# Optimization experiments

Hardware: AMD Instinct MI355X
Metric: run time of the kernel (lower is better)

Reference implementation:

```python
import jax, jax.numpy as jnp
import numpy as np

WS = 8           # window_size
OV = 4           # overlap = int(window_size * overlap_ratio)
OS = WS + 2 * OV # overlap_size = 16
NH = 6           # num_heads
EPS = 1e-5


def setup_inputs() -> dict:
    key = jax.random.key(0)
    ks = jax.random.split(key, 5)
    B, C, H, W = 4, 192, 256, 256
    s = 0.02
    return {
        "x": jax.random.normal(ks[0], (B, C, H, W), jnp.float32),
        "norm_gamma": jnp.ones((C,), jnp.float32),
        "norm_beta": jnp.zeros((C,), jnp.float32),
        "Wq": s * jax.random.normal(ks[1], (C, C), jnp.float32),
        "bq": jnp.zeros((C,), jnp.float32),
        "Wkv": s * jax.random.normal(ks[2], (C, 2 * C), jnp.float32),
        "bkv": jnp.zeros((2 * C,), jnp.float32),
        "Wo": s * jax.random.normal(ks[3], (C, C), jnp.float32),
        "bo": jnp.zeros((C,), jnp.float32),
    }


def reference(x, norm_gamma, norm_beta, Wq, bq, Wkv, bkv, Wo, bo):
    B, C, H, W = x.shape
    hd = C // NH
    scale = hd ** (-0.5)
    nHw, nWw = H // WS, W // WS
    nW = nHw * nWw

    residual = x
    xn = jnp.transpose(x, (0, 2, 3, 1))  # (B,H,W,C)
    mu = xn.mean(-1, keepdims=True)
    var = xn.var(-1, keepdims=True)
    ln = (xn - mu) * jax.lax.rsqrt(var + EPS) * norm_gamma + norm_beta  # (B,H,W,C)

    # --- queries: non-overlapping windows (window_partition) ---
    q_win = ln.reshape(B, nHw, WS, nWw, WS, C)
    q_win = jnp.transpose(q_win, (0, 1, 3, 2, 4, 5)).reshape(B * nW, WS * WS, C)
    q = q_win @ Wq + bq  # (N, ws^2, C)

    # --- keys/values: overlapping patches (Unfold equivalent) ---
    xp = jnp.pad(ln, ((0, 0), (OV, OV), (OV, OV), (0, 0)))  # (B,H+2ov,W+2ov,C)
    ih = (jnp.arange(nHw) * WS)[:, None] + jnp.arange(OS)[None, :]  # (nHw, OS)
    iw = (jnp.arange(nWw) * WS)[:, None] + jnp.arange(OS)[None, :]  # (nWw, OS)
    # (B, nHw, nWw, OS, OS, C)
    patches = xp[:, ih[:, None, :, None], iw[None, :, None, :], :]
    kv_in = patches.reshape(B * nW, OS * OS, C)
    kv = kv_in @ Wkv + bkv  # (N, os^2, 2C)
    k, v = kv[..., :C], kv[..., C:]

    # --- multi-head attention per window ---
    qh = q.reshape(-1, WS * WS, NH, hd).transpose(0, 2, 1, 3)   # (N,nh,q,hd)
    kh = k.reshape(-1, OS * OS, NH, hd).transpose(0, 2, 1, 3)   # (N,nh,kv,hd)
    vh = v.reshape(-1, OS * OS, NH, hd).transpose(0, 2, 1, 3)
    attn = jax.nn.softmax(jnp.einsum("nhqd,nhkd->nhqk", qh * scale, kh), axis=-1)
    out = jnp.einsum("nhqk,nhkd->nhqd", attn, vh)
    out = out.transpose(0, 2, 1, 3).reshape(-1, WS * WS, C)
    out = out @ Wo + bo

    # --- window_reverse + residual ---
    out = out.reshape(B, nHw, nWw, WS, WS, C)
    out = jnp.transpose(out, (0, 1, 3, 2, 4, 5)).reshape(B, H, W, C)
    return jnp.transpose(out, (0, 3, 1, 2)) + residual
```

## Files before the change

kernel.cpp:

```cpp
#include <hip/hip_runtime.h>
#include <hip/hip_bf16.h>

typedef __bf16 bf16;
typedef __bf16 bf16x8 __attribute__((ext_vector_type(8)));
typedef float f32x4 __attribute__((ext_vector_type(4)));
typedef unsigned int u32x2 __attribute__((ext_vector_type(2)));
typedef unsigned int u32x4 __attribute__((ext_vector_type(4)));

#define DEVI static __device__ __forceinline__

static constexpr int Bn = 4, Cc = 192, Hh = 256, Wd = 256;
static constexpr int NHd = 6, HD = 32;
static constexpr int Mtot = Bn * Hh * Wd;
static constexpr float EPSv = 1e-5f;
static constexpr float SCQ = 0.2550629072427404f;

DEVI f32x4 mfma16(bf16x8 a, bf16x8 b, f32x4 c) {
    return __builtin_amdgcn_mfma_f32_16x16x32_bf16(a, b, c, 0, 0, 0);
}

DEVI f32x4 mfma16f8(long long a, long long b, f32x4 c) {
    return __builtin_amdgcn_mfma_f32_16x16x32_fp8_fp8(a, b, c, 0, 0, 0);
}

template <bool HIGH>
DEVI unsigned cvtpk_fp8(float lo, float hi, unsigned old) {
    return (unsigned)__builtin_amdgcn_cvt_pk_fp8_f32(lo, hi, (int)old, HIGH);
}

__global__ __launch_bounds__(256) void k_prep(const float* Wq, const float* Wkv,
                                              const float* Wo, bf16* WT,
                                              unsigned char* WoT8) {
    int idx = blockIdx.x * 256 + threadIdx.x;
    if (idx < 576 * 192) {
        int n = idx / 192, k = idx % 192;
        float v = (n < 192) ? Wq[k * 192 + n] * SCQ : Wkv[k * 384 + (n - 192)];
        WT[idx] = (bf16)v;
    } else if (idx < 576 * 192 + 192 * 192) {
        int j = idx - 576 * 192;
        int n = j / 192, k = j % 192;
        float w = Wo[k * 192 + n];
        WoT8[j] = (unsigned char)(cvtpk_fp8<false>(w, w, 0u) & 0xFFu);
    }
}

__global__ __launch_bounds__(256) void k_lnqkv(const float* __restrict__ x,
                                               const float* __restrict__ gamma,
                                               const float* __restrict__ beta,
                                               const bf16* __restrict__ WT,
                                               const float* __restrict__ bq,
                                               const float* __restrict__ bkv,
                                               unsigned char* __restrict__ QKV8) {
    constexpr int AS = 200;
    __shared__ __align__(16) bf16 A[64 * AS];
    __shared__ float red[2][4][64];
    __shared__ float sg[Cc], sbv[Cc];

    int tid = threadIdx.x;
    int q = tid >> 6, p = tid & 63;
    int base = blockIdx.x * 64;
    int b = base >> 16;
    int hw = base & 65535;
    int h = hw >> 8, w0 = hw & 255;
    if (tid < Cc) { sg[tid] = gamma[tid]; sbv[tid] = beta[tid]; }

    const float* xb = x + ((size_t)(b * Cc + q * 48) * Hh + h) * Wd + w0 + p;
    float xv[48];
#pragma unroll
    for (int i = 0; i < 48; ++i) xv[i] = xb[(size_t)i * Hh * Wd];
    float s = 0.f, s2 = 0.f;
#pragma unroll
    for (int i = 0; i < 48; ++i) { s += xv[i]; s2 += xv[i] * xv[i]; }
    red[0][q][p] = s; red[1][q][p] = s2;
    __syncthreads();
    float mu = (red[0][0][p] + red[0][1][p] + red[0][2][p] + red[0][3][p]) * (1.f / 192.f);
    float m2 = (red[1][0][p] + red[1][1][p] + red[1][2][p] + red[1][3][p]) * (1.f / 192.f);
    float rs = rsqrtf(m2 - mu * mu + EPSv);
#pragma unroll
    for (int i0 = 0; i0 < 48; i0 += 8) {
        bf16x8 o;
#pragma unroll
        for (int j = 0; j < 8; ++j) {
            int c = q * 48 + i0 + j;
            o[j] = (bf16)((xv[i0 + j] - mu) * rs * sg[c] + sbv[c]);
        }
        *(bf16x8*)&A[p * AS + q * 48 + i0] = o;
    }
    __syncthreads();

    int lane = tid & 63, l15 = lane & 15, g = lane >> 4;
    const bf16* Wbase = WT + (size_t)(q * 144 + l15) * Cc + g * 8;
#pragma unroll 1
    for (int nt = 0; nt < 9; ++nt) {
        f32x4 acc[4] = {};
        const bf16* wp = Wbase + (size_t)nt * 16 * Cc;
#pragma unroll
        for (int kk = 0; kk < 6; ++kk) {
            bf16x8 wb = *(const bf16x8*)(wp + kk * 32);
#pragma unroll
            for (int mt = 0; mt < 4; ++mt) {
                bf16x8 a = *(bf16x8*)&A[(mt * 16 + l15) * AS + kk * 32 + g * 8];
                acc[mt] = mfma16(wb, a, acc[mt]);
            }
        }
        int n0 = q * 144 + nt * 16 + g * 4;
        const float* bsrc = (n0 < 192) ? (bq + n0) : (bkv + n0 - 192);
        f32x4 b4 = *(const f32x4*)bsrc;
        if (n0 < 192) b4 *= SCQ;
        unsigned char* outp = QKV8 + (size_t)(n0 >> 5) * Mtot * HD + (n0 & 31);
#pragma unroll
        for (int mt = 0; mt < 4; ++mt) {
            unsigned pk = 0;
            pk = cvtpk_fp8<false>(acc[mt][0] + b4[0], acc[mt][1] + b4[1], pk);
            pk = cvtpk_fp8<true>(acc[mt][2] + b4[2], acc[mt][3] + b4[3], pk);
            *(unsigned*)(outp + (size_t)(base + mt * 16 + l15) * HD) = pk;
        }
    }
}

__global__ __launch_bounds__(128) void k_attn(const unsigned char* __restrict__ QKV8,
                                              const float* __restrict__ bkv,
                                              unsigned char* __restrict__ AO8) {
    constexpr int VS = 264;
    int bid = blockIdx.x;
    bid = (bid & 7) * 3072 + (bid >> 3);
    int head = bid >> 12;
    int win = bid & 4095;
    int b = win >> 10, wloc = win & 1023;
    int h0 = ((wloc >> 5) << 3), w0 = ((wloc & 31) << 3);
    bool interior = (h0 != 0) && (h0 != Hh - 8) && (w0 != 0) && (w0 != Wd - 8);

    int tid = threadIdx.x, wave = tid >> 6, lane = tid & 63;
    int l15 = lane & 15, g = lane >> 4;

    const unsigned char* Qh = QKV8 + (size_t)head * Mtot * HD;
    const unsigned char* Kh = QKV8 + (size_t)(6 + head) * Mtot * HD;
    const unsigned char* Vh = QKV8 + (size_t)(12 + head) * Mtot * HD;
    unsigned char* Oh = AO8 + (size_t)head * Mtot * HD;
    long long p00 = (long long)(b * Hh + h0 - 4) * Wd + (w0 - 4);

    __shared__ __align__(16) unsigned char VT8[32 * VS];

#pragma unroll
    for (int rr = 0; rr < 2; ++rr) {
        int r = tid + rr * 128;
        unsigned wv[8];
        if (interior) {
            const unsigned char* vr = Vh + (p00 + (r >> 4) * Wd + (r & 15)) * HD;
            u32x4 a0 = *(const u32x4*)(vr);
            u32x4 a1 = *(const u32x4*)(vr + 16);
#pragma unroll
            for (int w = 0; w < 4; ++w) { wv[w] = a0[w]; wv[w + 4] = a1[w]; }
        } else {
            int ph = h0 - 4 + (r >> 4), pw = w0 - 4 + (r & 15);
            bool ok = ((unsigned)ph < (unsigned)Hh) && ((unsigned)pw < (unsigned)Wd);
            long long pix = ok ? ((long long)(b * Hh + ph) * Wd + pw) : 0;
            const unsigned char* vr = Vh + pix * HD;
            u32x4 a0 = *(const u32x4*)(vr);
            u32x4 a1 = *(const u32x4*)(vr + 16);
            const float* vb = bkv + Cc + head * HD;
#pragma unroll
            for (int w = 0; w < 8; ++w) {
                unsigned bw = 0;
                bw = cvtpk_fp8<false>(vb[4 * w], vb[4 * w + 1], bw);
                bw = cvtpk_fp8<true>(vb[4 * w + 2], vb[4 * w + 3], bw);
                unsigned lw = (w < 4) ? a0[w] : a1[w - 4];
                wv[w] = ok ? lw : bw;
            }
        }
#pragma unroll
        for (int w = 0; w < 8; ++w) {
            unsigned word = wv[w];
            VT8[(4 * w + 0) * VS + r] = (unsigned char)(word);
            VT8[(4 * w + 1) * VS + r] = (unsigned char)(word >> 8);
            VT8[(4 * w + 2) * VS + r] = (unsigned char)(word >> 16);
            VT8[(4 * w + 3) * VS + r] = (unsigned char)(word >> 24);
        }
    }

    int qrA = wave * 32 + l15;
    int qrB = qrA + 16;
    size_t qpixA = (size_t)(b * Hh + h0 + (qrA >> 3)) * Wd + w0 + (qrA & 7);
    size_t qpixB = (size_t)(b * Hh + h0 + (qrB >> 3)) * Wd + w0 + (qrB & 7);
    long long aqA = *(const long long*)(Qh + qpixA * HD + g * 8);
    long long aqB = *(const long long*)(Qh + qpixB * HD + g * 8);
    __syncthreads();

    const f32x4 z = {0.f, 0.f, 0.f, 0.f};
    const unsigned char* kp = Kh + (p00 + l15) * HD + g * 8;
    float sa0 = 0.f, sa1 = 0.f, sa2 = 0.f, sa3 = 0.f;
    float sb0 = 0.f, sb1 = 0.f, sb2 = 0.f, sb3 = 0.f;
    unsigned pkA[16], pkB[16];
    long long kb = 0;
    bool colok = true;
    if (!interior) {
        unsigned kb0 = 0, kb1 = 0;
        const float* kbp = bkv + head * HD + g * 8;
        kb0 = cvtpk_fp8<false>(kbp[0], kbp[1], kb0);
        kb0 = cvtpk_fp8<true>(kbp[2], kbp[3], kb0);
        kb1 = cvtpk_fp8<false>(kbp[4], kbp[5], kb1);
        kb1 = cvtpk_fp8<true>(kbp[6], kbp[7], kb1);
        kb = (long long)(((unsigned long long)kb1 << 32) | kb0);
        colok = ((unsigned)(w0 - 4 + l15) < (unsigned)Wd);
    }
#pragma unroll 1
    for (int c = 0; c < 4; ++c) {
        f32x4 sA[4], sB[4];
        __builtin_amdgcn_s_setprio(1);
        if (interior) {
#pragma unroll
            for (int u = 0; u < 4; ++u) {
                long long kf = *(const long long*)(kp + (size_t)(c * 4 + u) * Wd * HD);
                sA[u] = mfma16f8(kf, aqA, z);
                sB[u] = mfma16f8(kf, aqB, z);
            }
        } else {
#pragma unroll
            for (int u = 0; u < 4; ++u) {
                int t = c * 4 + u;
                int ph = h0 - 4 + t;
                long long kf;
                if ((unsigned)ph < (unsigned)Hh) {
                    kf = *(const long long*)(kp + (size_t)t * Wd * HD);
                    kf = colok ? kf : kb;
                } else {
                    kf = kb;
                }
                sA[u] = mfma16f8(kf, aqA, z);
                sB[u] = mfma16f8(kf, aqB, z);
            }
        }
        __builtin_amdgcn_s_setprio(0);
#pragma unroll
        for (int u = 0; u < 4; ++u) {
            float a0 = __builtin_amdgcn_exp2f(sA[u][0]);
            float a1 = __builtin_amdgcn_exp2f(sA[u][1]);
            float a2 = __builtin_amdgcn_exp2f(sA[u][2]);
            float a3 = __builtin_amdgcn_exp2f(sA[u][3]);
            sa0 += a0; sa1 += a1; sa2 += a2; sa3 += a3;
            unsigned wA = 0;
            wA = cvtpk_fp8<false>(a0, a1, wA);
            wA = cvtpk_fp8<true>(a2, a3, wA);
            pkA[c * 4 + u] = wA;
            float b0 = __builtin_amdgcn_exp2f(sB[u][0]);
            float b1 = __builtin_amdgcn_exp2f(sB[u][1]);
            float b2 = __builtin_amdgcn_exp2f(sB[u][2]);
            float b3 = __builtin_amdgcn_exp2f(sB[u][3]);
            sb0 += b0; sb1 += b1; sb2 += b2; sb3 += b3;
            unsigned wB = 0;
            wB = cvtpk_fp8<false>(b0, b1, wB);
            wB = cvtpk_fp8<true>(b2, b3, wB);
            pkB[c * 4 + u] = wB;
        }
    }
    float sumA = (sa0 + sa1) + (sa2 + sa3);
    sumA += __shfl_xor(sumA, 16);
    sumA += __shfl_xor(sumA, 32);
    float invA = __builtin_amdgcn_rcpf(sumA);
    float sumB = (sb0 + sb1) + (sb2 + sb3);
    sumB += __shfl_xor(sumB, 16);
    sumB += __shfl_xor(sumB, 32);
    float invB = __builtin_amdgcn_rcpf(sumB);

    int srcA = l15 | ((2 * (g & 1)) << 4);
    int srcB = srcA + 16;
    bool ghi = (g >> 1) != 0;
#define PV_EPILOGUE(PK, INV, JT)                                                        \
    {                                                                                   \
        f32x4 o0 = z, o1 = z;                                                           \
        _Pragma("unroll")                                                               \
        for (int kk = 0; kk < 8; ++kk) {                                                \
            unsigned s0 = __shfl(PK[2 * kk], srcA);                                     \
            unsigned s1 = __shfl(PK[2 * kk + 1], srcA);                                 \
            unsigned s2 = __shfl(PK[2 * kk], srcB);                                     \
            unsigned s3 = __shfl(PK[2 * kk + 1], srcB);                                 \
            unsigned lo = ghi ? s1 : s0;                                                \
            unsigned hi = ghi ? s3 : s2;                                                \
            long long ap = (long long)(((unsigned long long)hi << 32) | lo);            \
            long long bv0 = *(const long long*)&VT8[l15 * VS + kk * 32 + g * 8];        \
            long long bv1 = *(const long long*)&VT8[(16 + l15) * VS + kk * 32 + g * 8]; \
            __builtin_amdgcn_s_setprio(1);                                              \
            o0 = mfma16f8(ap, bv0, o0);                                                 \
            o1 = mfma16f8(ap, bv1, o1);                                                 \
            __builtin_amdgcn_s_setprio(0);                                              \
        }                                                                               \
        float invr[4];                                                                  \
        _Pragma("unroll")                                                               \
        for (int r = 0; r < 4; ++r)                                                     \
            invr[r] = __shfl(INV, (lane & 48) | (g * 4 + r));                           \
        _Pragma("unroll")                                                               \
        for (int r = 0; r < 4; ++r) {                                                   \
            int row = wave * 32 + JT * 16 + g * 4 + r;                                  \
            size_t pix = (size_t)(b * Hh + h0 + (row >> 3)) * Wd + w0 + (row & 7);      \
            float v0 = o0[r] * invr[r];                                                 \
            float v1 = o1[r] * invr[r];                                                 \
            Oh[pix * HD + l15] = (unsigned char)(cvtpk_fp8<false>(v0, v0, 0u) & 0xFFu); \
            Oh[pix * HD + 16 + l15] = (unsigned char)(cvtpk_fp8<false>(v1, v1, 0u) & 0xFFu); \
        }                                                                               \
    }
    PV_EPILOGUE(pkA, invA, 0)
    PV_EPILOGUE(pkB, invB, 1)
#undef PV_EPILOGUE
}

__global__ __launch_bounds__(256) void k_out(const unsigned char* __restrict__ AO8,
                                             const unsigned char* __restrict__ WoT8,
                                             const float* __restrict__ bo,
                                             const float* __restrict__ x,
                                             float* __restrict__ out) {
    int row0 = blockIdx.x * 64;
    int tid = threadIdx.x, wave = tid >> 6, lane = tid & 63;
    int l15 = lane & 15, g = lane >> 4;
    int nb = wave * 48;
    f32x4 acc[4][3] = {};
    const unsigned char* Arow[4];
#pragma unroll
    for (int mt = 0; mt < 4; ++mt) Arow[mt] = AO8 + (size_t)(row0 + mt * 16 + l15) * HD + g * 8;
    const unsigned char* Wrow[3];
#pragma unroll
    for (int nt = 0; nt < 3; ++nt) Wrow[nt] = WoT8 + (size_t)(nb + nt * 16 + l15) * Cc + g * 8;
#pragma unroll
    for (int kk = 0; kk < 6; ++kk) {
        long long a[4];
#pragma unroll
        for (int mt = 0; mt < 4; ++mt)
            a[mt] = *(const long long*)(Arow[mt] + (size_t)kk * Mtot * HD);
#pragma unroll
        for (int nt = 0; nt < 3; ++nt) {
            long long bb = *(const long long*)(Wrow[nt] + kk * 32);
#pragma unroll
            for (int mt = 0; mt < 4; ++mt) acc[mt][nt] = mfma16f8(a[mt], bb, acc[mt][nt]);
        }
    }
    __shared__ float st[192 * 65];
#pragma unroll
    for (int nt = 0; nt < 3; ++nt) {
        float bval = bo[nb + nt * 16 + l15];
#pragma unroll
        for (int mt = 0; mt < 4; ++mt)
#pragma unroll
            for (int r = 0; r < 4; ++r) {
                int ccol = nb + nt * 16 + l15;
                int px = mt * 16 + g * 4 + r;
                st[ccol * 65 + px] = acc[mt][nt][r] + bval;
            }
    }
    __syncthreads();
    int bb2 = row0 / (Hh * Wd);
    int rem = row0 % (Hh * Wd);
    int h = rem / Wd, wstart = rem % Wd;
    for (int idx = tid; idx < 192 * 64; idx += 256) {
        int cc = idx >> 6, px = idx & 63;
        size_t ga = ((size_t)(bb2 * Cc + cc) * Hh + h) * Wd + wstart + px;
        out[ga] = st[cc * 65 + px] + x[ga];
    }
}

extern "C" void kernel_launch(void* const* d_in, const int* in_sizes, int n_in,
                              void* d_out, int out_size, void* d_ws, size_t ws_size,
                              hipStream_t stream) {
    const float* x     = (const float*)d_in[0];
    const float* gamma = (const float*)d_in[1];
    const float* beta  = (const float*)d_in[2];
    const float* Wq    = (const float*)d_in[3];
    const float* bq    = (const float*)d_in[4];
    const float* Wkv   = (const float*)d_in[5];
    const float* bkv   = (const float*)d_in[6];
    const float* Wo    = (const float*)d_in[7];
    const float* bo    = (const float*)d_in[8];
    float* out = (float*)d_out;

    char* ws = (char*)d_ws;
    constexpr size_t P8  = (size_t)Mtot * HD;
    constexpr size_t QKV8SZ = 18 * P8;
    constexpr size_t AO8SZ  = 6 * P8;
    unsigned char* QKV8 = (unsigned char*)(ws);
    unsigned char* AO8  = (unsigned char*)(ws + QKV8SZ);
    bf16*          WT   = (bf16*)(ws + QKV8SZ + AO8SZ);
    unsigned char* WoT8 = (unsigned char*)(ws + QKV8SZ + AO8SZ + 221184);

    k_prep<<<576, 256, 0, stream>>>(Wq, Wkv, Wo, WT, WoT8);
    k_lnqkv<<<Mtot / 64, 256, 0, stream>>>(x, gamma, beta, WT, bq, bkv, QKV8);
    k_attn<<<4096 * NHd, 128, 0, stream>>>(QKV8, bkv, AO8);
    k_out<<<Mtot / 64, 256, 0, stream>>>(AO8, WoT8, bo, x, out);
}
```

Before: 403.5 us.

## Use fp8 MFMA for LN+QKV projection with full-row tiles per block

Switches the LayerNorm+QKV GEMM from bf16 to fp8 MFMA. Weights are pre-scaled by 16 and quantized to fp8, and the normalized activations are stored as fp8 in LDS. Each block now handles a full 256-pixel image row, with one thread computing per-pixel LN statistics over all channels, so the cross-wave reduction is gone and each weight fragment is reused across four times more pixels. The cost is a second read of x for normalization and lower precision for both activations and weights, which risks accuracy. Occupancy also drops because of the larger LDS footprint.

New measurement: 380.0 us. -5.8%, faster.

```diff
diff --git a/kernel.cpp b/kernel.cpp
--- a/kernel.cpp
+++ b/kernel.cpp
@@ -15,10 +15,6 @@
 static constexpr float EPSv = 1e-5f;
 static constexpr float SCQ = 0.2550629072427404f;
 
-DEVI f32x4 mfma16(bf16x8 a, bf16x8 b, f32x4 c) {
-    return __builtin_amdgcn_mfma_f32_16x16x32_bf16(a, b, c, 0, 0, 0);
-}
-
 DEVI f32x4 mfma16f8(long long a, long long b, f32x4 c) {
     return __builtin_amdgcn_mfma_f32_16x16x32_fp8_fp8(a, b, c, 0, 0, 0);
 }
@@ -29,13 +25,14 @@
 }
 
 __global__ __launch_bounds__(256) void k_prep(const float* Wq, const float* Wkv,
-                                              const float* Wo, bf16* WT,
+                                              const float* Wo, unsigned char* WT8,
                                               unsigned char* WoT8) {
     int idx = blockIdx.x * 256 + threadIdx.x;
     if (idx < 576 * 192) {
         int n = idx / 192, k = idx % 192;
-        float v = (n < 192) ? Wq[k * 192 + n] * SCQ : Wkv[k * 384 + (n - 192)];
-        WT[idx] = (bf16)v;
+        float v = (n < 192) ? Wq[k * 192 + n] * (SCQ * 16.f)
+                            : Wkv[k * 384 + (n - 192)] * 16.f;
+        WT8[idx] = (unsigned char)(cvtpk_fp8<false>(v, v, 0u) & 0xFFu);
     } else if (idx < 576 * 192 + 192 * 192) {
         int j = idx - 576 * 192;
         int n = j / 192, k = j % 192;
@@ -47,73 +44,79 @@
 __global__ __launch_bounds__(256) void k_lnqkv(const float* __restrict__ x,
                                                const float* __restrict__ gamma,
                                                const float* __restrict__ beta,
-                                               const bf16* __restrict__ WT,
+                                               const unsigned char* __restrict__ WT8,
                                                const float* __restrict__ bq,
                                                const float* __restrict__ bkv,
                                                unsigned char* __restrict__ QKV8) {
     constexpr int AS = 200;
-    __shared__ __align__(16) bf16 A[64 * AS];
-    __shared__ float red[2][4][64];
-    __shared__ float sg[Cc], sbv[Cc];
+    __shared__ __align__(16) unsigned char A[256 * AS];
 
     int tid = threadIdx.x;
-    int q = tid >> 6, p = tid & 63;
-    int base = blockIdx.x * 64;
-    int b = base >> 16;
-    int hw = base & 65535;
-    int h = hw >> 8, w0 = hw & 255;
-    if (tid < Cc) { sg[tid] = gamma[tid]; sbv[tid] = beta[tid]; }
-
-    const float* xb = x + ((size_t)(b * Cc + q * 48) * Hh + h) * Wd + w0 + p;
-    float xv[48];
-#pragma unroll
-    for (int i = 0; i < 48; ++i) xv[i] = xb[(size_t)i * Hh * Wd];
-    float s = 0.f, s2 = 0.f;
-#pragma unroll
-    for (int i = 0; i < 48; ++i) { s += xv[i]; s2 += xv[i] * xv[i]; }
-    red[0][q][p] = s; red[1][q][p] = s2;
+    int bid = blockIdx.x;
+    int b = bid >> 8, h = bid & 255;
+    const size_t cs = (size_t)Hh * Wd;
+    const float* xb = x + ((size_t)(b * Cc) * Hh + h) * Wd + tid;
+
+    float s0 = 0.f, s1 = 0.f, q0 = 0.f, q1 = 0.f;
+#pragma unroll 8
+    for (int c = 0; c < Cc; c += 2) {
+        float v0 = xb[(size_t)c * cs], v1 = xb[(size_t)(c + 1) * cs];
+        s0 += v0; q0 += v0 * v0;
+        s1 += v1; q1 += v1 * v1;
+    }
+    float mu = (s0 + s1) * (1.f / 192.f);
+    float m2 = (q0 + q1) * (1.f / 192.f);
+    float rs = rsqrtf(m2 - mu * mu + EPSv);
+
+#pragma unroll 4
+    for (int c = 0; c < Cc; c += 4) {
+        float v0 = (xb[(size_t)(c + 0) * cs] - mu) * rs * gamma[c + 0] + beta[c + 0];
+        float v1 = (xb[(size_t)(c + 1) * cs] - mu) * rs * gamma[c + 1] + beta[c + 1];
+        float v2 = (xb[(size_t)(c + 2) * cs] - mu) * rs * gamma[c + 2] + beta[c + 2];
+        float v3 = (xb[(size_t)(c + 3) * cs] - mu) * rs * gamma[c + 3] + beta[c + 3];
+        unsigned pk = 0;
+        pk = cvtpk_fp8<false>(v0, v1, pk);
+        pk = cvtpk_fp8<true>(v2, v3, pk);
+        *(unsigned*)&A[tid * AS + c] = pk;
+    }
     __syncthreads();
-    float mu = (red[0][0][p] + red[0][1][p] + red[0][2][p] + red[0][3][p]) * (1.f / 192.f);
-    float m2 = (red[1][0][p] + red[1][1][p] + red[1][2][p] + red[1][3][p]) * (1.f / 192.f);
-    float rs = rsqrtf(m2 - mu * mu + EPSv);
-#pragma unroll
-    for (int i0 = 0; i0 < 48; i0 += 8) {
-        bf16x8 o;
-#pragma unroll
-        for (int j = 0; j < 8; ++j) {
-            int c = q * 48 + i0 + j;
-            o[j] = (bf16)((xv[i0 + j] - mu) * rs * sg[c] + sbv[c]);
-        }
-        *(bf16x8*)&A[p * AS + q * 48 + i0] = o;
-    }
-    __syncthreads();
-
-    int lane = tid & 63, l15 = lane & 15, g = lane >> 4;
-    const bf16* Wbase = WT + (size_t)(q * 144 + l15) * Cc + g * 8;
+
+    int q = tid >> 6, lane = tid & 63, l15 = lane & 15, g = lane >> 4;
+    const unsigned char* Wbase = WT8 + (size_t)(q * 144 + l15) * Cc + g * 8;
+    size_t pixrow = ((size_t)(b * Hh) + h) * Wd;
 #pragma unroll 1
     for (int nt = 0; nt < 9; ++nt) {
-        f32x4 acc[4] = {};
-        const bf16* wp = Wbase + (size_t)nt * 16 * Cc;
-#pragma unroll
-        for (int kk = 0; kk < 6; ++kk) {
-            bf16x8 wb = *(const bf16x8*)(wp + kk * 32);
-#pragma unroll
-            for (int mt = 0; mt < 4; ++mt) {
-                bf16x8 a = *(bf16x8*)&A[(mt * 16 + l15) * AS + kk * 32 + g * 8];
-                acc[mt] = mfma16(wb, a, acc[mt]);
-            }
-        }
+        long long wf[6];
+        const unsigned char* wp = Wbase + (size_t)nt * 16 * Cc;
+#pragma unroll
+        for (int kk = 0; kk < 6; ++kk) wf[kk] = *(const long long*)(wp + kk * 32);
         int n0 = q * 144 + nt * 16 + g * 4;
         const float* bsrc = (n0 < 192) ? (bq + n0) : (bkv + n0 - 192);
         f32x4 b4 = *(const f32x4*)bsrc;
         if (n0 < 192) b4 *= SCQ;
         unsigned char* outp = QKV8 + (size_t)(n0 >> 5) * Mtot * HD + (n0 & 31);
-#pragma unroll
-        for (int mt = 0; mt < 4; ++mt) {
-            unsigned pk = 0;
-            pk = cvtpk_fp8<false>(acc[mt][0] + b4[0], acc[mt][1] + b4[1], pk);
-            pk = cvtpk_fp8<true>(acc[mt][2] + b4[2], acc[mt][3] + b4[3], pk);
-            *(unsigned*)(outp + (size_t)(base + mt * 16 + l15) * HD) = pk;
+#pragma unroll 1
+        for (int mtg = 0; mtg < 4; ++mtg) {
+            f32x4 acc[4] = {};
+#pragma unroll
+            for (int kk = 0; kk < 6; ++kk) {
+#pragma unroll
+                for (int m4 = 0; m4 < 4; ++m4) {
+                    int px = (mtg * 4 + m4) * 16 + l15;
+                    long long a = *(const long long*)&A[px * AS + kk * 32 + g * 8];
+                    acc[m4] = mfma16f8(wf[kk], a, acc[m4]);
+                }
+            }
+#pragma unroll
+            for (int m4 = 0; m4 < 4; ++m4) {
+                int px = (mtg * 4 + m4) * 16 + l15;
+                unsigned pk = 0;
+                pk = cvtpk_fp8<false>(fmaf(acc[m4][0], 0.0625f, b4[0]),
+                                      fmaf(acc[m4][1], 0.0625f, b4[1]), pk);
+                pk = cvtpk_fp8<true>(fmaf(acc[m4][2], 0.0625f, b4[2]),
+                                     fmaf(acc[m4][3], 0.0625f, b4[3]), pk);
+                *(unsigned*)(outp + (pixrow + px) * HD) = pk;
+            }
         }
     }
 }
@@ -376,11 +379,11 @@
     constexpr size_t AO8SZ  = 6 * P8;
     unsigned char* QKV8 = (unsigned char*)(ws);
     unsigned char* AO8  = (unsigned char*)(ws + QKV8SZ);
-    bf16*          WT   = (bf16*)(ws + QKV8SZ + AO8SZ);
-    unsigned char* WoT8 = (unsigned char*)(ws + QKV8SZ + AO8SZ + 221184);
-
-    k_prep<<<576, 256, 0, stream>>>(Wq, Wkv, Wo, WT, WoT8);
-    k_lnqkv<<<Mtot / 64, 256, 0, stream>>>(x, gamma, beta, WT, bq, bkv, QKV8);
+    unsigned char* WT8  = (unsigned char*)(ws + QKV8SZ + AO8SZ);
+    unsigned char* WoT8 = (unsigned char*)(ws + QKV8SZ + AO8SZ + 110592);
+
+    k_prep<<<576, 256, 0, stream>>>(Wq, Wkv, Wo, WT8, WoT8);
+    k_lnqkv<<<Mtot / 256, 256, 0, stream>>>(x, gamma, beta, WT8, bq, bkv, QKV8);
     k_attn<<<4096 * NHd, 128, 0, stream>>>(QKV8, bkv, AO8);
     k_out<<<Mtot / 64, 256, 0, stream>>>(AO8, WoT8, bo, x, out);
 }
```
